# Optimization experiments

Measured on AMD Instinct MI355X. Metric: run time of the kernel, lower is better.

Reference implementation:

```python
import jax, jax.numpy as jnp
import numpy as np

V, E, H, SC, SD = 32000, 512, 1024, 64, 128
B, T = 4, 1024


def setup_inputs() -> dict:
    key = jax.random.key(0)
    ks = jax.random.split(key, 32)
    g = lambda i, shape, s=0.02: (jax.random.normal(ks[i], shape, dtype=jnp.float32) * s)
    return {
        'input_ids': jax.random.randint(ks[0], (B, T), 0, V),
        'emb': g(1, (V, E)),
        'w_ih': g(2, (3 * H, E)), 'w_hh': g(3, (3 * H, H)),
        'b_ih': jnp.zeros((3 * H,), jnp.float32), 'b_hh': jnp.zeros((3 * H,), jnp.float32),
        'head_fc_w': g(4, (4 * E, H)), 'head_fc_b': jnp.zeros((4 * E,), jnp.float32),
        'head_proj_w': g(5, (E, 4 * E)), 'head_proj_b': jnp.zeros((E,), jnp.float32),
        'out_bias': jnp.zeros((V,), jnp.float32),
        'slot_init': g(6, (SC, SD)),
        'rq_w': g(7, (SD, H)), 'rq_b': jnp.zeros((SD,), jnp.float32),
        'wq_w': g(8, (SD, H)), 'wq_b': jnp.zeros((SD,), jnp.float32),
        'wv_w': g(9, (SD, H)), 'wv_b': jnp.zeros((SD,), jnp.float32),
        'wg_w': g(10, (SC, H)), 'wg_b': jnp.zeros((SC,), jnp.float32),
        'rm_w': g(11, (E, H)), 'rm_b': jnp.zeros((E,), jnp.float32),
        's2f_w': g(12, (E, SD)), 's2f_b': jnp.zeros((E,), jnp.float32),
    }


def _forward(input_ids, emb, w_ih, w_hh, b_ih, b_hh, head_fc_w, head_fc_b,
             head_proj_w, head_proj_b, out_bias, slot_init,
             rq_w, rq_b, wq_w, wq_b, wv_w, wv_b, wg_w, wg_b, rm_w, rm_b, s2f_w, s2f_b):
    x = emb[input_ids]                                  # [B,T,E]
    Bq, Tq = input_ids.shape
    Hh = w_hh.shape[1]
    # --- GRU (torch gate order r,z,n) ---
    gi = jnp.einsum('bte,ge->btg', x, w_ih) + b_ih      # [B,T,3H] precomputed input gates

    def gru_step(h, gi_t):
        gh = h @ w_hh.T + b_hh
        i_r, i_z, i_n = jnp.split(gi_t, 3, axis=-1)
        h_r, h_z, h_n = jnp.split(gh, 3, axis=-1)
        r = jax.nn.sigmoid(i_r + h_r)
        z = jax.nn.sigmoid(i_z + h_z)
        n = jnp.tanh(i_n + r * h_n)
        h = (1.0 - z) * n + z * h
        return h, h

    h0 = jnp.zeros((Bq, Hh), x.dtype)
    _, states = jax.lax.scan(gru_step, h0, jnp.swapaxes(gi, 0, 1))
    states = jnp.swapaxes(states, 0, 1)                 # [B,T,H]  (dropout=eval no-op)

    # --- slot memory recurrence: precompute all per-step projections ---
    rq = states @ rq_w.T + rq_b                         # [B,T,SD]
    wq = states @ wq_w.T + wq_b                         # [B,T,SD]
    wv = jnp.tanh(states @ wv_w.T + wv_b)               # [B,T,SD]
    wg = jax.nn.sigmoid(states @ wg_w.T + wg_b)         # [B,T,SC]

    def slot_step(slots, inp):
        rq_t, wq_t, wv_t, wg_t = inp
        read_attn = jax.nn.softmax(jnp.einsum('bd,bsd->bs', rq_t, slots), axis=-1)
        read_vec = jnp.einsum('bs,bsd->bd', read_attn, slots)
        write_attn = jax.nn.softmax(jnp.einsum('bd,bsd->bs', wq_t, slots), axis=-1)
        ws = (write_attn * wg_t)[..., None]             # [B,SC,1]
        slots = slots * (1.0 - ws) + wv_t[:, None, :] * ws
        return slots, read_vec

    slots0 = jnp.broadcast_to(slot_init, (Bq,) + slot_init.shape)
    seq = (jnp.swapaxes(rq, 0, 1), jnp.swapaxes(wq, 0, 1),
           jnp.swapaxes(wv, 0, 1), jnp.swapaxes(wg, 0, 1))
    _, read_vecs = jax.lax.scan(slot_step, slots0, seq)  # [T,B,SD]
    read_vecs = jnp.swapaxes(read_vecs, 0, 1)            # [B,T,SD]
    retrieved = read_vecs @ s2f_w.T + s2f_b              # [B,T,E]

    head = jnp.square(jax.nn.relu(states @ head_fc_w.T + head_fc_b))
    base = head @ head_proj_w.T + head_proj_b
    mixed = base + jax.nn.sigmoid(states @ rm_w.T + rm_b) * retrieved
    return mixed @ emb.T + out_bias                      # [B,T,V] tied logits


def reference(input_ids, emb, w_ih, w_hh, b_ih, b_hh, head_fc_w, head_fc_b,
              head_proj_w, head_proj_b, out_bias, slot_init,
              rq_w, rq_b, wq_w, wq_b, wv_w, wv_b, wg_w, wg_b, rm_w, rm_b, s2f_w, s2f_b):
    return _forward(input_ids, emb, w_ih, w_hh, b_ih, b_hh, head_fc_w, head_fc_b,
                    head_proj_w, head_proj_b, out_bias, slot_init,
                    rq_w, rq_b, wq_w, wq_b, wv_w, wv_b, wg_w, wg_b, rm_w, rm_b, s2f_w, s2f_b)
```

## Files before the change

### kernel.cpp

```cpp
#include <hip/hip_runtime.h>


#define DI __device__ __forceinline__

typedef _Float16 f16x2 __attribute__((ext_vector_type(2)));
typedef _Float16 f16x8 __attribute__((ext_vector_type(8)));
typedef float    f32x4 __attribute__((ext_vector_type(4)));

#define GLD16(gp, lp) __builtin_amdgcn_global_load_lds(                      \
    (const __attribute__((address_space(1))) void*)(gp),                     \
    (__attribute__((address_space(3))) void*)(lp), 16, 0, 0)

DI unsigned pack_h2(float a, float b) {
  f16x2 p; p[0] = (_Float16)a; p[1] = (_Float16)b;
  return __builtin_bit_cast(unsigned, p);
}
DI float sigmoid_acc(float x) { return 1.f / (1.f + expf(-x)); }

template <int EPI>
__global__ __launch_bounds__(256) void k_gemm_bt(
    const _Float16* __restrict__ A, const _Float16* __restrict__ B,
    const float* __restrict__ bias, float* __restrict__ C,
    _Float16* __restrict__ aux, int N, int K)
{
  __shared__ __attribute__((aligned(16))) _Float16 Ah[128 * 64];
  __shared__ __attribute__((aligned(16))) _Float16 Bh[128 * 64];
  const int tid = threadIdx.x;
  const int wv = tid >> 6, ln = tid & 63;
  const int bm = blockIdx.y << 7, bn = blockIdx.x << 7;
  const int wm = (wv >> 1) << 6, wn = (wv & 1) << 6;
  const int lrow = ln & 15, lk = ln >> 4;
  const int srow = ln >> 3, sseg = ln & 7;

  f32x4 acc[4][4];
#pragma unroll
  for (int i = 0; i < 4; ++i)
#pragma unroll
    for (int j = 0; j < 4; ++j) acc[i][j] = (f32x4){0.f, 0.f, 0.f, 0.f};

  for (int kt = 0; kt < K; kt += 64) {
#pragma unroll
    for (int c = 0; c < 4; ++c) {
      int ch = (wv << 2) + c;
      int row = (ch << 3) + srow;
      int seg = sseg ^ (row & 7);
      GLD16(A + (size_t)(bm + row) * K + kt + (seg << 3), &Ah[ch << 9]);
      GLD16(B + (size_t)(bn + row) * K + kt + (seg << 3), &Bh[ch << 9]);
    }
    __syncthreads();
#pragma unroll
    for (int ks = 0; ks < 2; ++ks) {
      f16x8 af[4], bf[4];
#pragma unroll
      for (int i = 0; i < 4; ++i) {
        int row = wm + (i << 4) + lrow;
        int phys = ((ks << 2) + lk) ^ (row & 7);
        af[i] = *(const f16x8*)&Ah[(row << 6) + (phys << 3)];
      }
#pragma unroll
      for (int j = 0; j < 4; ++j) {
        int row = wn + (j << 4) + lrow;
        int phys = ((ks << 2) + lk) ^ (row & 7);
        bf[j] = *(const f16x8*)&Bh[(row << 6) + (phys << 3)];
      }
#pragma unroll
      for (int i = 0; i < 4; ++i)
#pragma unroll
        for (int j = 0; j < 4; ++j)
          acc[i][j] = __builtin_amdgcn_mfma_f32_16x16x32_f16(af[i], bf[j], acc[i][j], 0, 0, 0);
    }
    __syncthreads();
  }
#pragma unroll
  for (int i = 0; i < 4; ++i) {
    int row0 = bm + wm + (i << 4) + (lk << 2);
#pragma unroll
    for (int j = 0; j < 4; ++j) {
      int col = bn + wn + (j << 4) + lrow;
      float bv = bias[col];
#pragma unroll
      for (int r = 0; r < 4; ++r) {
        float v = acc[i][j][r] + bv;
        if (EPI == 1) {
          if (col < 256) {  }
          else if (col < 384) v = tanhf(v);
          else if (col < 448) v = sigmoid_acc(v);
          else if (col < 2496) { v = fmaxf(v, 0.f); v = v * v; }
          else v = sigmoid_acc(v);
        }
        C[(size_t)(row0 + r) * N + col] = v;
        if (EPI == 1 && col >= 448 && col < 2496)
          aux[(size_t)(row0 + r) * 2048 + (col - 448)] = (_Float16)v;
      }
    }
  }
}

__global__ __launch_bounds__(256) void k_gru(
    const float* __restrict__ gi,
    const float* __restrict__ w_hh,
    const float* __restrict__ b_hh,
    float* __restrict__ h_steps,
    _Float16* __restrict__ states_h)
{
  const int tid = threadIdx.x;
  const int w = tid >> 6, l = tid & 63;
  const int xid = blockIdx.x & 7, sid = blockIdx.x >> 3;
  const int chain = xid >> 1;
  const int slice = ((xid & 1) << 5) + sid;
  const int u0 = slice << 4;
  const int G = (w << 2) + (l >> 4);
  const int j = l & 15;

  __shared__ __attribute__((aligned(16))) unsigned hh2[512];
  __shared__ float rsum[48];
  __shared__ float bhhs[48];

  unsigned wreg[3][32];
#pragma unroll
  for (int c = 0; c < 3; ++c) {
    int i = G * 3 + c;
    int R = ((i >> 4) << 10) + u0 + (i & 15);
    const float* wrow = w_hh + ((size_t)R << 10);
#pragma unroll
    for (int q = 0; q < 16; ++q) {
      float4 v = *(const float4*)(wrow + (q << 6) + (j << 2));
      wreg[c][2 * q]     = pack_h2(v.x, v.y);
      wreg[c][2 * q + 1] = pack_h2(v.z, v.w);
    }
  }
  if (tid < 48)
    bhhs[tid] = b_hh[((tid >> 4) << 10) + u0 + (tid & 15)];

  float h_old = 0.f;
  float g_r = 0.f, g_z = 0.f, g_n = 0.f;
  if (w == 0 && l < 16) {
    size_t gb = ((size_t)chain << 10) * 3072;
    g_r = gi[gb + u0 + l];
    g_z = gi[gb + 1024 + u0 + l];
    g_n = gi[gb + 2048 + u0 + l];
  }
  __syncthreads();

  for (int t = 0; t < 1024; ++t) {
    size_t bt = ((size_t)chain << 10) + t;
    if (t == 0) {
      hh2[2 * tid] = 0u; hh2[2 * tid + 1] = 0u;
    } else {
      const unsigned long long* hp =
          (const unsigned long long*)(h_steps + ((bt - 1) << 10));
      unsigned long long d0, d1;
      for (;;) {
        d0 = __hip_atomic_load(hp + 2 * tid, __ATOMIC_RELAXED, __HIP_MEMORY_SCOPE_AGENT);
        if ((unsigned)d0 != 0xAAAAAAAAu && (unsigned)(d0 >> 32) != 0xAAAAAAAAu) break;
        __builtin_amdgcn_s_sleep(1);
      }
      for (;;) {
        d1 = __hip_atomic_load(hp + 2 * tid + 1, __ATOMIC_RELAXED, __HIP_MEMORY_SCOPE_AGENT);
        if ((unsigned)d1 != 0xAAAAAAAAu && (unsigned)(d1 >> 32) != 0xAAAAAAAAu) break;
        __builtin_amdgcn_s_sleep(1);
      }
      float f0 = __uint_as_float((unsigned)d0);
      float f1 = __uint_as_float((unsigned)(d0 >> 32));
      float f2 = __uint_as_float((unsigned)d1);
      float f3 = __uint_as_float((unsigned)(d1 >> 32));
      hh2[2 * tid]     = pack_h2(f0, f1);
      hh2[2 * tid + 1] = pack_h2(f2, f3);
    }
    __syncthreads();

    float a0 = 0.f, a1 = 0.f, a2 = 0.f;
#pragma unroll
    for (int q = 0; q < 16; ++q) {
      uint2 hu = *(const uint2*)&hh2[(q << 5) + (j << 1)];
      f16x2 h0 = __builtin_bit_cast(f16x2, hu.x);
      f16x2 h1 = __builtin_bit_cast(f16x2, hu.y);
      a0 = __builtin_amdgcn_fdot2(__builtin_bit_cast(f16x2, wreg[0][2 * q]),     h0, a0, false);
      a0 = __builtin_amdgcn_fdot2(__builtin_bit_cast(f16x2, wreg[0][2 * q + 1]), h1, a0, false);
      a1 = __builtin_amdgcn_fdot2(__builtin_bit_cast(f16x2, wreg[1][2 * q]),     h0, a1, false);
      a1 = __builtin_amdgcn_fdot2(__builtin_bit_cast(f16x2, wreg[1][2 * q + 1]), h1, a1, false);
      a2 = __builtin_amdgcn_fdot2(__builtin_bit_cast(f16x2, wreg[2][2 * q]),     h0, a2, false);
      a2 = __builtin_amdgcn_fdot2(__builtin_bit_cast(f16x2, wreg[2][2 * q + 1]), h1, a2, false);
    }
#pragma unroll
    for (int m = 1; m <= 8; m <<= 1) {
      a0 += __shfl_xor(a0, m, 64);
      a1 += __shfl_xor(a1, m, 64);
      a2 += __shfl_xor(a2, m, 64);
    }
    if (j == 0) { rsum[G * 3] = a0; rsum[G * 3 + 1] = a1; rsum[G * 3 + 2] = a2; }
    __syncthreads();

    if (w == 0 && l < 16) {
      float sr = rsum[l] + bhhs[l];
      float sz = rsum[16 + l] + bhhs[16 + l];
      float sn = rsum[32 + l] + bhhs[32 + l];
      float r = 1.f / (1.f + __expf(-(g_r + sr)));
      float z = 1.f / (1.f + __expf(-(g_z + sz)));
      float arg = g_n + r * sn;
      float n = 1.f - 2.f / (__expf(2.f * arg) + 1.f);
      h_old = (1.f - z) * n + z * h_old;
      __hip_atomic_store(h_steps + (bt << 10) + u0 + l, h_old,
                         __ATOMIC_RELAXED, __HIP_MEMORY_SCOPE_AGENT);
      states_h[(bt << 10) + u0 + l] = (_Float16)h_old;
      if (t + 1 < 1024) {
        size_t gb = (bt + 1) * 3072;
        g_r = gi[gb + u0 + l];
        g_z = gi[gb + 1024 + u0 + l];
        g_n = gi[gb + 2048 + u0 + l];
      }
    }
    __syncthreads();
  }
}

__global__ __launch_bounds__(256) void k_slot(
    const float* __restrict__ act2,
    const float* __restrict__ slot_init,
    _Float16* __restrict__ rv_h)
{
  const int b = blockIdx.x;
  const int tid = threadIdx.x;
  __shared__ float slots[64 * 129];
  __shared__ __attribute__((aligned(16))) float lin[448];
  __shared__ float pr[256], pw[256];
  __shared__ float ar[64], aws[64];
  __shared__ float rvp[256];

  for (int k = tid; k < 8192; k += 256)
    slots[(k >> 7) * 129 + (k & 127)] = slot_init[k];

  float2 pf = {0.f, 0.f};
  if (tid < 224)
    pf = *(const float2*)(act2 + ((size_t)b << 10) * 3072 + (tid << 1));

  const int s_ = tid & 63, q_ = tid >> 6;

  for (int t = 0; t < 1024; ++t) {
    size_t bt = ((size_t)b << 10) + t;
    if (tid < 224) *(float2*)&lin[tid << 1] = pf;
    __syncthreads();
    if (tid < 224 && t + 1 < 1024)
      pf = *(const float2*)(act2 + (bt + 1) * 3072 + (tid << 1));

    {
      const float* srow = &slots[s_ * 129 + (q_ << 5)];
      const float* qv  = &lin[q_ << 5];
      const float* wqv = &lin[128 + (q_ << 5)];
      float p0 = 0.f, p1 = 0.f;
#pragma unroll
      for (int i = 0; i < 32; ++i) {
        float sv = srow[i];
        p0 += sv * qv[i];
        p1 += sv * wqv[i];
      }
      pr[(q_ << 6) + s_] = p0;
      pw[(q_ << 6) + s_] = p1;
    }
    __syncthreads();
    if (tid < 64) {
      float lg = pr[tid] + pr[64 + tid] + pr[128 + tid] + pr[192 + tid];
      float mx = lg;
#pragma unroll
      for (int m = 1; m <= 32; m <<= 1) mx = fmaxf(mx, __shfl_xor(mx, m, 64));
      float e = __expf(lg - mx);
      float sm = e;
#pragma unroll
      for (int m = 1; m <= 32; m <<= 1) sm += __shfl_xor(sm, m, 64);
      ar[tid] = e / sm;
    } else if (tid < 128) {
      int s = tid - 64;
      float lg = pw[s] + pw[64 + s] + pw[128 + s] + pw[192 + s];
      float mx = lg;
#pragma unroll
      for (int m = 1; m <= 32; m <<= 1) mx = fmaxf(mx, __shfl_xor(mx, m, 64));
      float e = __expf(lg - mx);
      float sm = e;
#pragma unroll
      for (int m = 1; m <= 32; m <<= 1) sm += __shfl_xor(sm, m, 64);
      aws[s] = (e / sm) * lin[384 + s];
    }
    __syncthreads();
    {
      int d = tid & 127, sh = tid >> 7;
      float rv = 0.f;
#pragma unroll
      for (int i = 0; i < 32; ++i) {
        int s = (sh << 5) + i;
        rv += ar[s] * slots[s * 129 + d];
      }
      rvp[(sh << 7) + d] = rv;
    }
    __syncthreads();
    if (tid < 128)
      rv_h[(bt << 7) + tid] = (_Float16)(rvp[tid] + rvp[128 + tid]);
    {
      int s = tid >> 2, c = tid & 3;
      float wsv = aws[s];
      float fr = 1.f - wsv;
      const float* wvq = &lin[256 + (c << 5)];
      float* srw = &slots[s * 129 + (c << 5)];
#pragma unroll
      for (int i = 0; i < 32; ++i)
        srw[i] = srw[i] * fr + wvq[i] * wsv;
    }
    __syncthreads();
  }
}

__global__ void k_f32_to_f16_v8(const float* __restrict__ src,
                                _Float16* __restrict__ dst, int n8) {
  int i = blockIdx.x * 256 + threadIdx.x;
  if (i >= n8) return;
  float4 a = *(const float4*)(src + ((size_t)i << 3));
  float4 b = *(const float4*)(src + ((size_t)i << 3) + 4);
  f16x8 o;
  o[0] = (_Float16)a.x; o[1] = (_Float16)a.y; o[2] = (_Float16)a.z; o[3] = (_Float16)a.w;
  o[4] = (_Float16)b.x; o[5] = (_Float16)b.y; o[6] = (_Float16)b.z; o[7] = (_Float16)b.w;
  *(f16x8*)(dst + ((size_t)i << 3)) = o;
}

__global__ void k_build_wcat(const float* __restrict__ rq, const float* __restrict__ wq,
                             const float* __restrict__ wvw, const float* __restrict__ wg,
                             const float* __restrict__ hf, const float* __restrict__ rm,
                             _Float16* __restrict__ out) {
  int idx = blockIdx.x * 256 + threadIdx.x;
  if (idx >= 3072 * 1024) return;
  int row = idx >> 10, col = idx & 1023;
  float v;
  if      (row < 128)  v = rq[row * 1024 + col];
  else if (row < 256)  v = wq[(row - 128) * 1024 + col];
  else if (row < 384)  v = wvw[(row - 256) * 1024 + col];
  else if (row < 448)  v = wg[(row - 384) * 1024 + col];
  else if (row < 2496) v = hf[(row - 448) * 1024 + col];
  else if (row < 3008) v = rm[(row - 2496) * 1024 + col];
  else v = 0.f;
  out[idx] = (_Float16)v;
}

__global__ void k_build_biascat(const float* __restrict__ rq, const float* __restrict__ wq,
                                const float* __restrict__ wvb, const float* __restrict__ wg,
                                const float* __restrict__ hf, const float* __restrict__ rm,
                                float* __restrict__ out) {
  int r = blockIdx.x * 256 + threadIdx.x;
  if (r >= 3072) return;
  float v;
  if      (r < 128)  v = rq[r];
  else if (r < 256)  v = wq[r - 128];
  else if (r < 384)  v = wvb[r - 256];
  else if (r < 448)  v = wg[r - 384];
  else if (r < 2496) v = hf[r - 448];
  else if (r < 3008) v = rm[r - 2496];
  else v = 0.f;
  out[r] = v;
}

__global__ void k_gather_x(const int* __restrict__ ids,
                           const _Float16* __restrict__ emb_h,
                           _Float16* __restrict__ x_h) {
  int row = blockIdx.x;
  int id = ids[row];
  const unsigned* s = (const unsigned*)(emb_h + ((size_t)id << 9));
  unsigned* d = (unsigned*)(x_h + ((size_t)row << 9));
  d[threadIdx.x] = s[threadIdx.x];
}

__global__ void k_fill_u32(unsigned* __restrict__ p, unsigned v, int n) {
  int i = blockIdx.x * 256 + threadIdx.x;
  if (i < n) p[i] = v;
}

__global__ void k_mix(const float* __restrict__ base, const float* __restrict__ act2,
                      const float* __restrict__ retr, _Float16* __restrict__ out) {
  int idx = blockIdx.x * 256 + threadIdx.x;
  if (idx >= 4096 * 512) return;
  int r = idx >> 9, e = idx & 511;
  float v = base[idx] + act2[(size_t)r * 3072 + 2496 + e] * retr[idx];
  out[idx] = (_Float16)v;
}

extern "C" void kernel_launch(void* const* d_in, const int* in_sizes, int n_in,
                              void* d_out, int out_size, void* d_ws, size_t ws_size,
                              hipStream_t stream)
{
  const int*   ids   = (const int*)d_in[0];
  const float* emb   = (const float*)d_in[1];
  const float* w_ih  = (const float*)d_in[2];
  const float* w_hh  = (const float*)d_in[3];
  const float* b_ih  = (const float*)d_in[4];
  const float* b_hh  = (const float*)d_in[5];
  const float* hf_w  = (const float*)d_in[6];
  const float* hf_b  = (const float*)d_in[7];
  const float* hp_w  = (const float*)d_in[8];
  const float* hp_b  = (const float*)d_in[9];
  const float* o_b   = (const float*)d_in[10];
  const float* sinit = (const float*)d_in[11];
  const float* rq_w  = (const float*)d_in[12];
  const float* rq_b  = (const float*)d_in[13];
  const float* wq_w  = (const float*)d_in[14];
  const float* wq_b  = (const float*)d_in[15];
  const float* wv_w  = (const float*)d_in[16];
  const float* wv_b  = (const float*)d_in[17];
  const float* wg_w  = (const float*)d_in[18];
  const float* wg_b  = (const float*)d_in[19];
  const float* rm_w  = (const float*)d_in[20];
  const float* rm_b  = (const float*)d_in[21];
  const float* s2f_w = (const float*)d_in[22];
  const float* s2f_b = (const float*)d_in[23];

  char* ws = (char*)d_ws;
  _Float16* emb_h   = (_Float16*)(ws + 0);
  _Float16* x_h     = (_Float16*)(ws + 32768000);
  _Float16* wih_h   = (_Float16*)(ws + 36962304);
  _Float16* wcat_h  = (_Float16*)(ws + 40108032);
  float*    biascat = (float*)   (ws + 46399488);
  _Float16* hpw_h   = (_Float16*)(ws + 46411776);
  _Float16* s2f_h   = (_Float16*)(ws + 48508928);
  float*    gi      = (float*)   (ws + 48640000);
  float*    act2    = (float*)   (ws + 98971648);
  float*    h_steps = (float*)   (ws + 149303296);
  _Float16* states_h= (_Float16*)(ws + 166080512);
  _Float16* headh   = (_Float16*)(ws + 174469120);
  _Float16* rv_h    = (_Float16*)(ws + 191246336);
  float*    base    = (float*)   (ws + 192294912);
  float*    retr    = (float*)   (ws + 200683520);
  _Float16* mixed_h = (_Float16*)(ws + 209072128);
  float* out = (float*)d_out;

  k_f32_to_f16_v8<<<8000, 256, 0, stream>>>(emb, emb_h, 2048000);
  k_f32_to_f16_v8<<<768, 256, 0, stream>>>(w_ih, wih_h, 196608);
  k_f32_to_f16_v8<<<512, 256, 0, stream>>>(hp_w, hpw_h, 131072);
  k_f32_to_f16_v8<<<32, 256, 0, stream>>>(s2f_w, s2f_h, 8192);
  k_build_wcat<<<12288, 256, 0, stream>>>(rq_w, wq_w, wv_w, wg_w, hf_w, rm_w, wcat_h);
  k_build_biascat<<<12, 256, 0, stream>>>(rq_b, wq_b, wv_b, wg_b, hf_b, rm_b, biascat);
  k_gather_x<<<4096, 256, 0, stream>>>(ids, emb_h, x_h);
  k_fill_u32<<<16384, 256, 0, stream>>>((unsigned*)h_steps, 0xAAAAAAAAu, 4194304);

  k_gemm_bt<0><<<dim3(24, 32), 256, 0, stream>>>(x_h, wih_h, b_ih, gi, nullptr, 3072, 512);

  k_gru<<<256, 256, 0, stream>>>(gi, w_hh, b_hh, h_steps, states_h);

  k_gemm_bt<1><<<dim3(24, 32), 256, 0, stream>>>(states_h, wcat_h, biascat, act2, headh, 3072, 1024);

  k_slot<<<4, 256, 0, stream>>>(act2, sinit, rv_h);

  k_gemm_bt<0><<<dim3(4, 32), 256, 0, stream>>>(headh, hpw_h, hp_b, base, nullptr, 512, 2048);
  k_gemm_bt<0><<<dim3(4, 32), 256, 0, stream>>>(rv_h, s2f_h, s2f_b, retr, nullptr, 512, 128);
  k_mix<<<8192, 256, 0, stream>>>(base, act2, retr, mixed_h);
  k_gemm_bt<0><<<dim3(250, 32), 256, 0, stream>>>(mixed_h, emb_h, o_b, out, nullptr, 32000, 512);
}
```

Before: 5.010 ms.

## Exchange GRU state as packed fp16 and restructure slot-memory step loop

The GRU blocks now publish each new hidden state as packed fp16 pairs to a half-size exchange buffer. Consumers then need one 64-bit polled load per thread and no fp32-to-fp16 conversion, and the trailing barrier per step is removed. The fp16 dot products are split across two accumulators to break the dependency chain. The slot kernel is restructured: double-buffered step inputs, an XOR-swizzled slot layout instead of padding, a single fused pass that computes the read vector and updates the slots, and deferred reduction of the previous step's read vector. Together these cut barriers per step in both serial recurrences, at the cost of a sentinel-collision tweak on packed values and more delicate cross-step buffer reuse.

```diff
diff --git a/kernel.cpp b/kernel.cpp
--- a/kernel.cpp
+++ b/kernel.cpp
@@ -82,7 +82,7 @@
       for (int r = 0; r < 4; ++r) {
         float v = acc[i][j][r] + bv;
         if (EPI == 1) {
-          if (col < 256) {  }
+          if (col < 256) { }
           else if (col < 384) v = tanhf(v);
           else if (col < 448) v = sigmoid_acc(v);
           else if (col < 2496) { v = fmaxf(v, 0.f); v = v * v; }
@@ -100,7 +100,7 @@
     const float* __restrict__ gi,
     const float* __restrict__ w_hh,
     const float* __restrict__ b_hh,
-    float* __restrict__ h_steps,
+    unsigned* __restrict__ h16,
     _Float16* __restrict__ states_h)
 {
   const int tid = threadIdx.x;
@@ -148,40 +148,39 @@
       hh2[2 * tid] = 0u; hh2[2 * tid + 1] = 0u;
     } else {
       const unsigned long long* hp =
-          (const unsigned long long*)(h_steps + ((bt - 1) << 10));
-      unsigned long long d0, d1;
+          (const unsigned long long*)(h16 + ((bt - 1) << 9));
+      unsigned long long d;
       for (;;) {
-        d0 = __hip_atomic_load(hp + 2 * tid, __ATOMIC_RELAXED, __HIP_MEMORY_SCOPE_AGENT);
-        if ((unsigned)d0 != 0xAAAAAAAAu && (unsigned)(d0 >> 32) != 0xAAAAAAAAu) break;
+        d = __hip_atomic_load(hp + tid, __ATOMIC_RELAXED, __HIP_MEMORY_SCOPE_AGENT);
+        if ((unsigned)d != 0xAAAAAAAAu && (unsigned)(d >> 32) != 0xAAAAAAAAu) break;
         __builtin_amdgcn_s_sleep(1);
       }
-      for (;;) {
-        d1 = __hip_atomic_load(hp + 2 * tid + 1, __ATOMIC_RELAXED, __HIP_MEMORY_SCOPE_AGENT);
-        if ((unsigned)d1 != 0xAAAAAAAAu && (unsigned)(d1 >> 32) != 0xAAAAAAAAu) break;
-        __builtin_amdgcn_s_sleep(1);
-      }
-      float f0 = __uint_as_float((unsigned)d0);
-      float f1 = __uint_as_float((unsigned)(d0 >> 32));
-      float f2 = __uint_as_float((unsigned)d1);
-      float f3 = __uint_as_float((unsigned)(d1 >> 32));
-      hh2[2 * tid]     = pack_h2(f0, f1);
-      hh2[2 * tid + 1] = pack_h2(f2, f3);
-    }
-    __syncthreads();
-
-    float a0 = 0.f, a1 = 0.f, a2 = 0.f;
-#pragma unroll
-    for (int q = 0; q < 16; ++q) {
-      uint2 hu = *(const uint2*)&hh2[(q << 5) + (j << 1)];
-      f16x2 h0 = __builtin_bit_cast(f16x2, hu.x);
-      f16x2 h1 = __builtin_bit_cast(f16x2, hu.y);
-      a0 = __builtin_amdgcn_fdot2(__builtin_bit_cast(f16x2, wreg[0][2 * q]),     h0, a0, false);
-      a0 = __builtin_amdgcn_fdot2(__builtin_bit_cast(f16x2, wreg[0][2 * q + 1]), h1, a0, false);
-      a1 = __builtin_amdgcn_fdot2(__builtin_bit_cast(f16x2, wreg[1][2 * q]),     h0, a1, false);
-      a1 = __builtin_amdgcn_fdot2(__builtin_bit_cast(f16x2, wreg[1][2 * q + 1]), h1, a1, false);
-      a2 = __builtin_amdgcn_fdot2(__builtin_bit_cast(f16x2, wreg[2][2 * q]),     h0, a2, false);
-      a2 = __builtin_amdgcn_fdot2(__builtin_bit_cast(f16x2, wreg[2][2 * q + 1]), h1, a2, false);
-    }
+      hh2[2 * tid]     = (unsigned)d;
+      hh2[2 * tid + 1] = (unsigned)(d >> 32);
+    }
+    __syncthreads();
+
+    float a0 = 0.f, a1 = 0.f, a2 = 0.f, a3 = 0.f, a4 = 0.f, a5 = 0.f;
+#pragma unroll
+    for (int q = 0; q < 16; q += 2) {
+      uint2 hA = *(const uint2*)&hh2[(q << 5) + (j << 1)];
+      uint2 hB = *(const uint2*)&hh2[((q + 1) << 5) + (j << 1)];
+      f16x2 hA0 = __builtin_bit_cast(f16x2, hA.x), hA1 = __builtin_bit_cast(f16x2, hA.y);
+      f16x2 hB0 = __builtin_bit_cast(f16x2, hB.x), hB1 = __builtin_bit_cast(f16x2, hB.y);
+      a0 = __builtin_amdgcn_fdot2(__builtin_bit_cast(f16x2, wreg[0][2 * q]),     hA0, a0, false);
+      a0 = __builtin_amdgcn_fdot2(__builtin_bit_cast(f16x2, wreg[0][2 * q + 1]), hA1, a0, false);
+      a3 = __builtin_amdgcn_fdot2(__builtin_bit_cast(f16x2, wreg[0][2 * q + 2]), hB0, a3, false);
+      a3 = __builtin_amdgcn_fdot2(__builtin_bit_cast(f16x2, wreg[0][2 * q + 3]), hB1, a3, false);
+      a1 = __builtin_amdgcn_fdot2(__builtin_bit_cast(f16x2, wreg[1][2 * q]),     hA0, a1, false);
+      a1 = __builtin_amdgcn_fdot2(__builtin_bit_cast(f16x2, wreg[1][2 * q + 1]), hA1, a1, false);
+      a4 = __builtin_amdgcn_fdot2(__builtin_bit_cast(f16x2, wreg[1][2 * q + 2]), hB0, a4, false);
+      a4 = __builtin_amdgcn_fdot2(__builtin_bit_cast(f16x2, wreg[1][2 * q + 3]), hB1, a4, false);
+      a2 = __builtin_amdgcn_fdot2(__builtin_bit_cast(f16x2, wreg[2][2 * q]),     hA0, a2, false);
+      a2 = __builtin_amdgcn_fdot2(__builtin_bit_cast(f16x2, wreg[2][2 * q + 1]), hA1, a2, false);
+      a5 = __builtin_amdgcn_fdot2(__builtin_bit_cast(f16x2, wreg[2][2 * q + 2]), hB0, a5, false);
+      a5 = __builtin_amdgcn_fdot2(__builtin_bit_cast(f16x2, wreg[2][2 * q + 3]), hB1, a5, false);
+    }
+    a0 += a3; a1 += a4; a2 += a5;
 #pragma unroll
     for (int m = 1; m <= 8; m <<= 1) {
       a0 += __shfl_xor(a0, m, 64);
@@ -200,9 +199,14 @@
       float arg = g_n + r * sn;
       float n = 1.f - 2.f / (__expf(2.f * arg) + 1.f);
       h_old = (1.f - z) * n + z * h_old;
-      __hip_atomic_store(h_steps + (bt << 10) + u0 + l, h_old,
-                         __ATOMIC_RELAXED, __HIP_MEMORY_SCOPE_AGENT);
-      states_h[(bt << 10) + u0 + l] = (_Float16)h_old;
+      float hpart = __shfl_xor(h_old, 1, 64);
+      if ((l & 1) == 0) {
+        unsigned pk = pack_h2(h_old, hpart);
+        ((unsigned*)states_h)[(bt << 9) + (u0 >> 1) + (l >> 1)] = pk;
+        if (pk == 0xAAAAAAAAu) pk ^= 1u;
+        __hip_atomic_store(&h16[(bt << 9) + (u0 >> 1) + (l >> 1)], pk,
+                           __ATOMIC_RELAXED, __HIP_MEMORY_SCOPE_AGENT);
+      }
       if (t + 1 < 1024) {
         size_t gb = (bt + 1) * 3072;
         g_r = gi[gb + u0 + l];
@@ -210,7 +214,6 @@
         g_n = gi[gb + 2048 + u0 + l];
       }
     }
-    __syncthreads();
   }
 }
 
@@ -221,45 +224,50 @@
 {
   const int b = blockIdx.x;
   const int tid = threadIdx.x;
-  __shared__ float slots[64 * 129];
-  __shared__ __attribute__((aligned(16))) float lin[448];
-  __shared__ float pr[256], pw[256];
+  __shared__ __attribute__((aligned(16))) float S[64 * 128];
+  __shared__ __attribute__((aligned(16))) float lin[2][456];
+  __shared__ float pr[4 * 65], pw[4 * 65];
   __shared__ float ar[64], aws[64];
-  __shared__ float rvp[256];
-
-  for (int k = tid; k < 8192; k += 256)
-    slots[(k >> 7) * 129 + (k & 127)] = slot_init[k];
-
+  __shared__ __attribute__((aligned(16))) float rvp[8 * 128];
+
+  for (int k = tid; k < 8192; k += 256) {
+    int s = k >> 7, d = k & 127;
+    S[(s << 7) + ((((d >> 2) ^ (s & 7))) << 2) + (d & 3)] = slot_init[k];
+  }
+
+  const size_t arow = (size_t)b << 10;
   float2 pf = {0.f, 0.f};
-  if (tid < 224)
-    pf = *(const float2*)(act2 + ((size_t)b << 10) * 3072 + (tid << 1));
-
-  const int s_ = tid & 63, q_ = tid >> 6;
+  if (tid < 224) {
+    float2 v0 = *(const float2*)(act2 + arow * 3072 + (tid << 1));
+    *(float2*)&lin[0][tid << 1] = v0;
+    pf = *(const float2*)(act2 + (arow + 1) * 3072 + (tid << 1));
+  }
+  const int q_ = tid >> 6, s_ = tid & 63;
+  const int oct = tid >> 5, dc = tid & 31;
+  __syncthreads();
 
   for (int t = 0; t < 1024; ++t) {
-    size_t bt = ((size_t)b << 10) + t;
-    if (tid < 224) *(float2*)&lin[tid << 1] = pf;
-    __syncthreads();
-    if (tid < 224 && t + 1 < 1024)
-      pf = *(const float2*)(act2 + (bt + 1) * 3072 + (tid << 1));
-
+    const int buf = t & 1;
     {
-      const float* srow = &slots[s_ * 129 + (q_ << 5)];
-      const float* qv  = &lin[q_ << 5];
-      const float* wqv = &lin[128 + (q_ << 5)];
-      float p0 = 0.f, p1 = 0.f;
-#pragma unroll
-      for (int i = 0; i < 32; ++i) {
-        float sv = srow[i];
-        p0 += sv * qv[i];
-        p1 += sv * wqv[i];
-      }
-      pr[(q_ << 6) + s_] = p0;
-      pw[(q_ << 6) + s_] = p1;
-    }
-    __syncthreads();
+      const float4* Srow = (const float4*)&S[s_ << 7];
+      const float4* rq4 = (const float4*)&lin[buf][q_ << 5];
+      const float4* wq4 = (const float4*)&lin[buf][128 + (q_ << 5)];
+      float pa = 0.f, pb = 0.f;
+#pragma unroll
+      for (int i = 0; i < 8; ++i) {
+        float4 v = Srow[(q_ << 3) + (i ^ (s_ & 7))];
+        float4 a = rq4[i];
+        float4 c = wq4[i];
+        pa += v.x * a.x + v.y * a.y + v.z * a.z + v.w * a.w;
+        pb += v.x * c.x + v.y * c.y + v.z * c.z + v.w * c.w;
+      }
+      pr[q_ * 65 + s_] = pa;
+      pw[q_ * 65 + s_] = pb;
+    }
+    __syncthreads();
+
     if (tid < 64) {
-      float lg = pr[tid] + pr[64 + tid] + pr[128 + tid] + pr[192 + tid];
+      float lg = pr[tid] + pr[65 + tid] + pr[130 + tid] + pr[195 + tid];
       float mx = lg;
 #pragma unroll
       for (int m = 1; m <= 32; m <<= 1) mx = fmaxf(mx, __shfl_xor(mx, m, 64));
@@ -270,7 +278,7 @@
       ar[tid] = e / sm;
     } else if (tid < 128) {
       int s = tid - 64;
-      float lg = pw[s] + pw[64 + s] + pw[128 + s] + pw[192 + s];
+      float lg = pw[s] + pw[65 + s] + pw[130 + s] + pw[195 + s];
       float mx = lg;
 #pragma unroll
       for (int m = 1; m <= 32; m <<= 1) mx = fmaxf(mx, __shfl_xor(mx, m, 64));
@@ -278,33 +286,58 @@
       float sm = e;
 #pragma unroll
       for (int m = 1; m <= 32; m <<= 1) sm += __shfl_xor(sm, m, 64);
-      aws[s] = (e / sm) * lin[384 + s];
-    }
-    __syncthreads();
+      aws[s] = (e / sm) * lin[buf][384 + s];
+    } else if (tid < 160 && t > 0) {
+      int d4 = tid - 128;
+      float x = 0.f, y = 0.f, z = 0.f, w = 0.f;
+#pragma unroll
+      for (int o = 0; o < 8; ++o) {
+        float4 v = *(const float4*)&rvp[(o << 7) + (d4 << 2)];
+        x += v.x; y += v.y; z += v.z; w += v.w;
+      }
+      uint2 pk; pk.x = pack_h2(x, y); pk.y = pack_h2(z, w);
+      *(uint2*)(rv_h + ((arow + (t - 1)) << 7) + (d4 << 2)) = pk;
+    }
+    __syncthreads();
+
+    if (tid < 224) {
+      *(float2*)&lin[buf ^ 1][tid << 1] = pf;
+      if (t + 2 < 1024)
+        pf = *(const float2*)(act2 + (arow + t + 2) * 3072 + (tid << 1));
+    }
     {
-      int d = tid & 127, sh = tid >> 7;
-      float rv = 0.f;
-#pragma unroll
-      for (int i = 0; i < 32; ++i) {
-        int s = (sh << 5) + i;
-        rv += ar[s] * slots[s * 129 + d];
-      }
-      rvp[(sh << 7) + d] = rv;
-    }
-    __syncthreads();
-    if (tid < 128)
-      rv_h[(bt << 7) + tid] = (_Float16)(rvp[tid] + rvp[128 + tid]);
-    {
-      int s = tid >> 2, c = tid & 3;
-      float wsv = aws[s];
-      float fr = 1.f - wsv;
-      const float* wvq = &lin[256 + (c << 5)];
-      float* srw = &slots[s * 129 + (c << 5)];
-#pragma unroll
-      for (int i = 0; i < 32; ++i)
-        srw[i] = srw[i] * fr + wvq[i] * wsv;
-    }
-    __syncthreads();
+      float4 wv4 = *(const float4*)&lin[buf][256 + (dc << 2)];
+      float rx = 0.f, ry = 0.f, rz = 0.f, rw = 0.f;
+      const int s0 = oct << 3;
+#pragma unroll
+      for (int i = 0; i < 8; ++i) {
+        int s = s0 + i;
+        float a = ar[s];
+        float wsv = aws[s];
+        float fr = 1.f - wsv;
+        float4* p = (float4*)&S[s << 7] + (dc ^ (s & 7));
+        float4 v = *p;
+        rx += a * v.x; ry += a * v.y; rz += a * v.z; rw += a * v.w;
+        v.x = v.x * fr + wv4.x * wsv;
+        v.y = v.y * fr + wv4.y * wsv;
+        v.z = v.z * fr + wv4.z * wsv;
+        v.w = v.w * fr + wv4.w * wsv;
+        *p = v;
+      }
+      float4 out; out.x = rx; out.y = ry; out.z = rz; out.w = rw;
+      *(float4*)&rvp[(oct << 7) + (dc << 2)] = out;
+    }
+    __syncthreads();
+  }
+  if (tid < 32) {
+    float x = 0.f, y = 0.f, z = 0.f, w = 0.f;
+#pragma unroll
+    for (int o = 0; o < 8; ++o) {
+      float4 v = *(const float4*)&rvp[(o << 7) + (tid << 2)];
+      x += v.x; y += v.y; z += v.z; w += v.w;
+    }
+    uint2 pk; pk.x = pack_h2(x, y); pk.y = pack_h2(z, w);
+    *(uint2*)(rv_h + ((arow + 1023) << 7) + (tid << 2)) = pk;
   }
 }
 
@@ -418,13 +451,14 @@
   _Float16* s2f_h   = (_Float16*)(ws + 48508928);
   float*    gi      = (float*)   (ws + 48640000);
   float*    act2    = (float*)   (ws + 98971648);
-  float*    h_steps = (float*)   (ws + 149303296);
+  unsigned* h16     = (unsigned*)(ws + 149303296);
   _Float16* states_h= (_Float16*)(ws + 166080512);
   _Float16* headh   = (_Float16*)(ws + 174469120);
   _Float16* rv_h    = (_Float16*)(ws + 191246336);
   float*    base    = (float*)   (ws + 192294912);
   float*    retr    = (float*)   (ws + 200683520);
   _Float16* mixed_h = (_Float16*)(ws + 209072128);
+
   float* out = (float*)d_out;
 
   k_f32_to_f16_v8<<<8000, 256, 0, stream>>>(emb, emb_h, 2048000);
@@ -434,16 +468,12 @@
   k_build_wcat<<<12288, 256, 0, stream>>>(rq_w, wq_w, wv_w, wg_w, hf_w, rm_w, wcat_h);
   k_build_biascat<<<12, 256, 0, stream>>>(rq_b, wq_b, wv_b, wg_b, hf_b, rm_b, biascat);
   k_gather_x<<<4096, 256, 0, stream>>>(ids, emb_h, x_h);
-  k_fill_u32<<<16384, 256, 0, stream>>>((unsigned*)h_steps, 0xAAAAAAAAu, 4194304);
+  k_fill_u32<<<8192, 256, 0, stream>>>(h16, 0xAAAAAAAAu, 2097152);
 
   k_gemm_bt<0><<<dim3(24, 32), 256, 0, stream>>>(x_h, wih_h, b_ih, gi, nullptr, 3072, 512);
-
-  k_gru<<<256, 256, 0, stream>>>(gi, w_hh, b_hh, h_steps, states_h);
-
+  k_gru<<<256, 256, 0, stream>>>(gi, w_hh, b_hh, h16, states_h);
   k_gemm_bt<1><<<dim3(24, 32), 256, 0, stream>>>(states_h, wcat_h, biascat, act2, headh, 3072, 1024);
-
   k_slot<<<4, 256, 0, stream>>>(act2, sinit, rv_h);
-
   k_gemm_bt<0><<<dim3(4, 32), 256, 0, stream>>>(headh, hpw_h, hp_b, base, nullptr, 512, 2048);
   k_gemm_bt<0><<<dim3(4, 32), 256, 0, stream>>>(rv_h, s2f_h, s2f_b, retr, nullptr, 512, 128);
   k_mix<<<8192, 256, 0, stream>>>(base, act2, retr, mixed_h);
```

After: 4.111 ms. 17.9% less time.
